# Performance work log

Hardware: AMD Instinct MI355X
Metric: run time of the kernel (lower is better)

Reference implementation:

```python
import jax, jax.numpy as jnp
import numpy as np

EPS = 1e-5


def _layer_norm(x, gamma, beta):
    mu = jnp.mean(x, axis=-1, keepdims=True)
    var = jnp.var(x, axis=-1, keepdims=True)
    return (x - mu) * jax.lax.rsqrt(var + EPS) * gamma + beta


def setup_inputs() -> dict:
    key = jax.random.key(0)
    B, I, H = 4096, 1024, 1024
    ks = jax.random.split(key, 6)
    x = jax.random.normal(ks[0], (B, I), dtype=jnp.float32)
    h = jax.random.normal(ks[1], (B, H), dtype=jnp.float32)
    c = jax.random.normal(ks[2], (B, H), dtype=jnp.float32)
    # nn.Linear(I+H, 4H): weight [4H, I+H], bias [4H]
    bound = 1.0 / np.sqrt(I + H)
    W = jax.random.uniform(ks[3], (4 * H, I + H), minval=-bound, maxval=bound, dtype=jnp.float32)
    b = jax.random.uniform(ks[4], (4 * H,), minval=-bound, maxval=bound, dtype=jnp.float32)
    inp = {"x": x, "h": h, "c": c, "W": W, "b": b}
    for name in ("i", "f", "g", "o", "c"):
        inp[f"ln_{name}_g"] = jnp.ones((H,), dtype=jnp.float32)
        inp[f"ln_{name}_b"] = jnp.zeros((H,), dtype=jnp.float32)
    return inp


def reference(x, h, c, W, b, ln_i_g, ln_i_b, ln_f_g, ln_f_b, ln_g_g, ln_g_b,
              ln_o_g, ln_o_b, ln_c_g, ln_c_b):
    H = h.shape[-1]
    xh = jnp.concatenate([x, h], axis=-1)              # [B, I+H]
    gates = xh @ W.T + b                               # [B, 4H]
    i_raw, f_raw, g_raw, o_raw = jnp.split(gates, 4, axis=-1)
    i = jax.nn.sigmoid(_layer_norm(i_raw, ln_i_g, ln_i_b))
    f = jax.nn.sigmoid(_layer_norm(f_raw, ln_f_g, ln_f_b))
    g = jnp.tanh(_layer_norm(g_raw, ln_g_g, ln_g_b))
    o = jax.nn.sigmoid(_layer_norm(o_raw, ln_o_g, ln_o_b))
    c_new = f * c + i * g
    h_new = o * jnp.tanh(_layer_norm(c_new, ln_c_g, ln_c_b))
    return (h_new, c_new)
```

## Files before the change

kernel.cpp:

```cpp
#include <hip/hip_runtime.h>
#include <hip/hip_bf16.h>

#define B_ROWS 4096
#define H_DIM  1024
#define K_DIM  2048
#define N_DIM  4096
#define NT     32

typedef __attribute__((ext_vector_type(8))) short bf16x8;
typedef __attribute__((ext_vector_type(4))) float f32x4;

__device__ __forceinline__ unsigned short f2bf(float f) {
  union { float f; unsigned int u; } v; v.f = f;
  unsigned int u = v.u;
  return (unsigned short)((u + 0x7fffu + ((u >> 16) & 1u)) >> 16);
}
__device__ __forceinline__ float bf2f(unsigned short u) {
  union { unsigned int u; float f; } v; v.u = ((unsigned int)u) << 16;
  return v.f;
}

__device__ __forceinline__ void gload_lds16(const void* g, void* l) {
  __builtin_amdgcn_global_load_lds(
      (const __attribute__((address_space(1))) void*)g,
      (__attribute__((address_space(3))) void*)l, 16, 0, 0);
}

__global__ __launch_bounds__(256) void pack_a_kernel(
    const float* __restrict__ x, const float* __restrict__ h,
    unsigned short* __restrict__ out) {
  int t = blockIdx.x * 256 + threadIdx.x;
  int e = t * 4;
  int row = e >> 11;
  int col = e & 2047;
  const float* src = (col < 1024) ? (x + (size_t)row * 1024 + col)
                                  : (h + (size_t)row * 1024 + (col - 1024));
  float4 v = *(const float4*)src;
  ushort4 o;
  o.x = f2bf(v.x); o.y = f2bf(v.y); o.z = f2bf(v.z); o.w = f2bf(v.w);
  *(ushort4*)(out + e) = o;
}

__global__ __launch_bounds__(256) void pack_w_kernel(
    const float* __restrict__ W, unsigned short* __restrict__ out) {
  int t = blockIdx.x * 256 + threadIdx.x;
  int e = t * 4;
  float4 v = *(const float4*)(W + e);
  ushort4 o;
  o.x = f2bf(v.x); o.y = f2bf(v.y); o.z = f2bf(v.z); o.w = f2bf(v.w);
  *(ushort4*)(out + e) = o;
}


#define STAGE(g, kt, dst) do {                              \
    gload_lds16((g) + (size_t)(kt) * 64, (dst));            \
    gload_lds16((g) + (size_t)(kt) * 64 + 32, (dst) + 1024); } while (0)

#define WAIT_LGKM0() do {                                   \
    asm volatile("s_waitcnt lgkmcnt(0)" ::: "memory");      \
    __builtin_amdgcn_sched_barrier(0); } while (0)

__global__ __launch_bounds__(512, 2) void gemm_kernel(
    const unsigned short* __restrict__ A, const unsigned short* __restrict__ W,
    const float* __restrict__ bias, unsigned short* __restrict__ C) {
  __shared__ __align__(16) char lds[131072];

  const int tid = threadIdx.x;
  const int w = tid >> 6, l = tid & 63;
  const int wm = w >> 2, wn = w & 3;
  const int bm = blockIdx.y * 256, bn = blockIdx.x * 256;

  const int lofs = (((l & 15) * 64) + ((l >> 4) * 16)) ^ ((l & 8) << 2);
  const int lane_r = (l >> 2) & 15;
  const int lane_c = ((l & 3) * 8) ^ (((l >> 5) & 1) * 16);

  const int rbA0 = w + (w & 4);
  const int rbA1 = rbA0 + 4;
  const int rbB0 = ((w >> 1) << 2) + (w & 1);
  const int rbB1 = rbB0 + 2;

  const unsigned short* gA0 = A + (size_t)(bm + rbA0 * 16 + lane_r) * K_DIM + lane_c;
  const unsigned short* gA1 = A + (size_t)(bm + rbA1 * 16 + lane_r) * K_DIM + lane_c;
  const unsigned short* gB0 = W + (size_t)(bn + rbB0 * 16 + lane_r) * K_DIM + lane_c;
  const unsigned short* gB1 = W + (size_t)(bn + rbB1 * 16 + lane_r) * K_DIM + lane_c;

  char* const L0 = lds;
  char* const L1 = lds + 65536;

  f32x4 acc[8][4];
#pragma unroll
  for (int i = 0; i < 8; ++i)
#pragma unroll
    for (int j = 0; j < 4; ++j) acc[i][j] = (f32x4)0.0f;

  STAGE(gA0, 0, L0 + rbA0 * 2048);
  STAGE(gB0, 0, L0 + 32768 + rbB0 * 2048);
  STAGE(gB1, 0, L0 + 32768 + rbB1 * 2048);
  STAGE(gA1, 0, L0 + rbA1 * 2048);
  STAGE(gA0, 1, L1 + rbA0 * 2048);
  STAGE(gB0, 1, L1 + 32768 + rbB0 * 2048);
  STAGE(gB1, 1, L1 + 32768 + rbB1 * 2048);
  asm volatile("s_waitcnt vmcnt(6)" ::: "memory");
  __builtin_amdgcn_s_barrier();

  bf16x8 a[4][2], b0[2][2], b1[2][2];

#pragma unroll 2
  for (int t = 0; t < NT; ++t) {
    const int buf = t & 1;
    char* const Lc = lds + buf * 65536;
    char* const Ln = lds + (buf ^ 1) * 65536;
    const char* const LA = Lc;
    const char* const LB = Lc + 32768;
    const int kt1 = (t + 1) & (NT - 1);
    const int kt2 = (t + 2) & (NT - 1);

#pragma unroll
    for (int mi = 0; mi < 4; ++mi)
#pragma unroll
      for (int kk = 0; kk < 2; ++kk)
        a[mi][kk] = *(const bf16x8*)(LA + (((wm * 8 + mi) * 2 + kk) << 10) + lofs);
#pragma unroll
    for (int ni = 0; ni < 2; ++ni)
#pragma unroll
      for (int kk = 0; kk < 2; ++kk)
        b0[ni][kk] = *(const bf16x8*)(LB + (((wn * 4 + ni) * 2 + kk) << 10) + lofs);
    STAGE(gA1, kt1, Ln + rbA1 * 2048);
    asm volatile("s_waitcnt lgkmcnt(8)" ::: "memory");
    __builtin_amdgcn_s_barrier();
    WAIT_LGKM0();
    __builtin_amdgcn_s_setprio(1);
#pragma unroll
    for (int mi = 0; mi < 4; ++mi)
#pragma unroll
      for (int ni = 0; ni < 2; ++ni)
#pragma unroll
        for (int kk = 0; kk < 2; ++kk)
          acc[mi][ni] = __builtin_amdgcn_mfma_f32_16x16x32_bf16(
              a[mi][kk], b0[ni][kk], acc[mi][ni], 0, 0, 0);
    __builtin_amdgcn_s_setprio(0);
    __builtin_amdgcn_s_barrier();

#pragma unroll
    for (int ni = 0; ni < 2; ++ni)
#pragma unroll
      for (int kk = 0; kk < 2; ++kk)
        b1[ni][kk] = *(const bf16x8*)(LB + (((wn * 4 + 2 + ni) * 2 + kk) << 10) + lofs);
    STAGE(gA0, kt2, Lc + rbA0 * 2048);
    __builtin_amdgcn_s_barrier();
    WAIT_LGKM0();
    __builtin_amdgcn_s_setprio(1);
#pragma unroll
    for (int mi = 0; mi < 4; ++mi)
#pragma unroll
      for (int ni = 0; ni < 2; ++ni)
#pragma unroll
        for (int kk = 0; kk < 2; ++kk)
          acc[mi][2 + ni] = __builtin_amdgcn_mfma_f32_16x16x32_bf16(
              a[mi][kk], b1[ni][kk], acc[mi][2 + ni], 0, 0, 0);
    __builtin_amdgcn_s_setprio(0);
    __builtin_amdgcn_s_barrier();

#pragma unroll
    for (int mi = 0; mi < 4; ++mi)
#pragma unroll
      for (int kk = 0; kk < 2; ++kk)
        a[mi][kk] = *(const bf16x8*)(LA + (((wm * 8 + 4 + mi) * 2 + kk) << 10) + lofs);
    STAGE(gB0, kt2, Lc + 32768 + rbB0 * 2048);
    __builtin_amdgcn_s_barrier();
    WAIT_LGKM0();
    __builtin_amdgcn_s_setprio(1);
#pragma unroll
    for (int mi = 0; mi < 4; ++mi)
#pragma unroll
      for (int ni = 0; ni < 2; ++ni)
#pragma unroll
        for (int kk = 0; kk < 2; ++kk)
          acc[4 + mi][2 + ni] = __builtin_amdgcn_mfma_f32_16x16x32_bf16(
              a[mi][kk], b1[ni][kk], acc[4 + mi][2 + ni], 0, 0, 0);
    __builtin_amdgcn_s_setprio(0);
    __builtin_amdgcn_s_barrier();

    STAGE(gB1, kt2, Lc + 32768 + rbB1 * 2048);
    asm volatile("s_waitcnt vmcnt(6)" ::: "memory");
    __builtin_amdgcn_s_barrier();
    __builtin_amdgcn_s_setprio(1);
#pragma unroll
    for (int mi = 0; mi < 4; ++mi)
#pragma unroll
      for (int ni = 0; ni < 2; ++ni)
#pragma unroll
        for (int kk = 0; kk < 2; ++kk)
          acc[4 + mi][ni] = __builtin_amdgcn_mfma_f32_16x16x32_bf16(
              a[mi][kk], b0[ni][kk], acc[4 + mi][ni], 0, 0, 0);
    __builtin_amdgcn_s_setprio(0);
    __builtin_amdgcn_s_barrier();
  }

  const int lm = l & 15, lq = l >> 4;
  float bv[4];
#pragma unroll
  for (int ni = 0; ni < 4; ++ni) bv[ni] = bias[bn + wn * 64 + ni * 16 + lm];
  unsigned short* Cb = C + (size_t)(bm + wm * 128) * N_DIM + bn + wn * 64;
#pragma unroll
  for (int mi = 0; mi < 8; ++mi)
#pragma unroll
    for (int j = 0; j < 4; ++j) {
      const size_t rofs = (size_t)(mi * 16 + lq * 4 + j) * N_DIM;
#pragma unroll
      for (int ni = 0; ni < 4; ++ni)
        Cb[rofs + ni * 16 + lm] = f2bf(acc[mi][ni][j] + bv[ni]);
    }
}

__device__ __forceinline__ float2 blk_sum2(float s, float q, float* red,
                                           int wid, int lane) {
#pragma unroll
  for (int o = 32; o >= 1; o >>= 1) {
    s += __shfl_xor(s, o, 64);
    q += __shfl_xor(q, o, 64);
  }
  __syncthreads();
  if (lane == 0) { red[wid * 2] = s; red[wid * 2 + 1] = q; }
  __syncthreads();
  s = red[0] + red[2] + red[4] + red[6];
  q = red[1] + red[3] + red[5] + red[7];
  return make_float2(s, q);
}

__device__ __forceinline__ float sigmoidf_(float x) {
  return 1.0f / (1.0f + __expf(-x));
}
__device__ __forceinline__ float tanhf_(float x) {
  return 1.0f - 2.0f / (__expf(2.0f * x) + 1.0f);
}

__global__ __launch_bounds__(256) void ln_lstm_kernel(
    const unsigned short* __restrict__ gates, const float* __restrict__ cprev,
    const float* __restrict__ g_i, const float* __restrict__ b_i,
    const float* __restrict__ g_f, const float* __restrict__ b_f,
    const float* __restrict__ g_g, const float* __restrict__ b_g,
    const float* __restrict__ g_o, const float* __restrict__ b_o,
    const float* __restrict__ g_c, const float* __restrict__ b_c,
    float* __restrict__ out) {
  const int b = blockIdx.x;
  const int t = threadIdx.x;
  const int wid = t >> 6, lane = t & 63;
  __shared__ float red[8];

  const unsigned short* grow = gates + (size_t)b * N_DIM;
  const int c0 = t * 4;

  float v[4][4];
#pragma unroll
  for (int g = 0; g < 4; g++) {
    ushort4 raw = *(const ushort4*)(grow + g * 1024 + c0);
    v[g][0] = bf2f(raw.x); v[g][1] = bf2f(raw.y);
    v[g][2] = bf2f(raw.z); v[g][3] = bf2f(raw.w);
  }

  const float4 gamma[4] = {*(const float4*)(g_i + c0), *(const float4*)(g_f + c0),
                           *(const float4*)(g_g + c0), *(const float4*)(g_o + c0)};
  const float4 beta[4]  = {*(const float4*)(b_i + c0), *(const float4*)(b_f + c0),
                           *(const float4*)(b_g + c0), *(const float4*)(b_o + c0)};

  float a[4][4];
#pragma unroll
  for (int g = 0; g < 4; g++) {
    float s = v[g][0] + v[g][1] + v[g][2] + v[g][3];
    float q = v[g][0]*v[g][0] + v[g][1]*v[g][1] + v[g][2]*v[g][2] + v[g][3]*v[g][3];
    float2 r = blk_sum2(s, q, red, wid, lane);
    float mu = r.x * (1.0f / 1024.0f);
    float var = r.y * (1.0f / 1024.0f) - mu * mu;
    float inv = rsqrtf(var + 1e-5f);
    const float* gm = (const float*)&gamma[g];
    const float* bt = (const float*)&beta[g];
#pragma unroll
    for (int j = 0; j < 4; j++) {
      float n = (v[g][j] - mu) * inv * gm[j] + bt[j];
      a[g][j] = (g == 2) ? tanhf_(n) : sigmoidf_(n);
    }
  }

  float4 cp = *(const float4*)(cprev + (size_t)b * 1024 + c0);
  const float* cpe = (const float*)&cp;
  float cn[4];
#pragma unroll
  for (int j = 0; j < 4; j++)
    cn[j] = a[1][j] * cpe[j] + a[0][j] * a[2][j];

  {
    float s = cn[0] + cn[1] + cn[2] + cn[3];
    float q = cn[0]*cn[0] + cn[1]*cn[1] + cn[2]*cn[2] + cn[3]*cn[3];
    float2 r = blk_sum2(s, q, red, wid, lane);
    float mu = r.x * (1.0f / 1024.0f);
    float var = r.y * (1.0f / 1024.0f) - mu * mu;
    float inv = rsqrtf(var + 1e-5f);
    float4 gm = *(const float4*)(g_c + c0);
    float4 bt = *(const float4*)(b_c + c0);
    const float* gme = (const float*)&gm;
    const float* bte = (const float*)&bt;
    float hn[4];
#pragma unroll
    for (int j = 0; j < 4; j++) {
      float n = (cn[j] - mu) * inv * gme[j] + bte[j];
      hn[j] = a[3][j] * tanhf_(n);
    }
    *(float4*)(out + (size_t)b * 1024 + c0) = make_float4(hn[0], hn[1], hn[2], hn[3]);
    *(float4*)(out + (size_t)B_ROWS * H_DIM + (size_t)b * 1024 + c0) =
        make_float4(cn[0], cn[1], cn[2], cn[3]);
  }
}

extern "C" void kernel_launch(void* const* d_in, const int* in_sizes, int n_in,
                              void* d_out, int out_size, void* d_ws,
                              size_t ws_size, hipStream_t stream) {
  const float* x    = (const float*)d_in[0];
  const float* h    = (const float*)d_in[1];
  const float* c    = (const float*)d_in[2];
  const float* W    = (const float*)d_in[3];
  const float* bias = (const float*)d_in[4];
  const float* ln_i_g = (const float*)d_in[5];
  const float* ln_i_b = (const float*)d_in[6];
  const float* ln_f_g = (const float*)d_in[7];
  const float* ln_f_b = (const float*)d_in[8];
  const float* ln_g_g = (const float*)d_in[9];
  const float* ln_g_b = (const float*)d_in[10];
  const float* ln_o_g = (const float*)d_in[11];
  const float* ln_o_b = (const float*)d_in[12];
  const float* ln_c_g = (const float*)d_in[13];
  const float* ln_c_b = (const float*)d_in[14];

  unsigned short* Abf = (unsigned short*)d_ws;
  unsigned short* Wbf = Abf + (size_t)B_ROWS * K_DIM;
  unsigned short* gates = Wbf + (size_t)N_DIM * K_DIM;

  pack_a_kernel<<<(B_ROWS * K_DIM) / (4 * 256), 256, 0, stream>>>(x, h, Abf);
  pack_w_kernel<<<(N_DIM * K_DIM) / (4 * 256), 256, 0, stream>>>(W, Wbf);

  dim3 ggrid(N_DIM / 256, B_ROWS / 256);
  gemm_kernel<<<ggrid, 512, 0, stream>>>(Abf, Wbf, bias, gates);

  ln_lstm_kernel<<<B_ROWS, 256, 0, stream>>>(
      gates, c, ln_i_g, ln_i_b, ln_f_g, ln_f_b, ln_g_g, ln_g_b,
      ln_o_g, ln_o_b, ln_c_g, ln_c_b, (float*)d_out);
}
```

Baseline: 104.6 us.

## Prefetch next-tile LDS fragments into double registers and merge pack kernels

```diff
diff --git a/kernel.cpp b/kernel.cpp
--- a/kernel.cpp
+++ b/kernel.cpp
@@ -26,29 +26,30 @@
       (__attribute__((address_space(3))) void*)l, 16, 0, 0);
 }
 
-__global__ __launch_bounds__(256) void pack_a_kernel(
+__global__ __launch_bounds__(256) void pack_kernel(
     const float* __restrict__ x, const float* __restrict__ h,
-    unsigned short* __restrict__ out) {
-  int t = blockIdx.x * 256 + threadIdx.x;
-  int e = t * 4;
-  int row = e >> 11;
-  int col = e & 2047;
-  const float* src = (col < 1024) ? (x + (size_t)row * 1024 + col)
-                                  : (h + (size_t)row * 1024 + (col - 1024));
-  float4 v = *(const float4*)src;
-  ushort4 o;
-  o.x = f2bf(v.x); o.y = f2bf(v.y); o.z = f2bf(v.z); o.w = f2bf(v.w);
-  *(ushort4*)(out + e) = o;
-}
-
-__global__ __launch_bounds__(256) void pack_w_kernel(
-    const float* __restrict__ W, unsigned short* __restrict__ out) {
-  int t = blockIdx.x * 256 + threadIdx.x;
-  int e = t * 4;
-  float4 v = *(const float4*)(W + e);
-  ushort4 o;
-  o.x = f2bf(v.x); o.y = f2bf(v.y); o.z = f2bf(v.z); o.w = f2bf(v.w);
-  *(ushort4*)(out + e) = o;
+    const float* __restrict__ W, unsigned short* __restrict__ Abf,
+    unsigned short* __restrict__ Wbf) {
+  int bid = blockIdx.x;
+  if (bid < 8192) {
+    int t = bid * 256 + threadIdx.x;
+    int e = t * 4;
+    int row = e >> 11;
+    int col = e & 2047;
+    const float* src = (col < 1024) ? (x + (size_t)row * 1024 + col)
+                                    : (h + (size_t)row * 1024 + (col - 1024));
+    float4 v = *(const float4*)src;
+    ushort4 o;
+    o.x = f2bf(v.x); o.y = f2bf(v.y); o.z = f2bf(v.z); o.w = f2bf(v.w);
+    *(ushort4*)(Abf + e) = o;
+  } else {
+    int t = (bid - 8192) * 256 + threadIdx.x;
+    int e = t * 4;
+    float4 v = *(const float4*)(W + e);
+    ushort4 o;
+    o.x = f2bf(v.x); o.y = f2bf(v.y); o.z = f2bf(v.z); o.w = f2bf(v.w);
+    *(ushort4*)(Wbf + e) = o;
+  }
 }
 
 
@@ -103,7 +104,18 @@
   asm volatile("s_waitcnt vmcnt(6)" ::: "memory");
   __builtin_amdgcn_s_barrier();
 
-  bf16x8 a[4][2], b0[2][2], b1[2][2];
+  bf16x8 a0[4][2], a1[4][2], b0[2][2], b1[2][2];
+
+#pragma unroll
+  for (int mi = 0; mi < 4; ++mi)
+#pragma unroll
+    for (int kk = 0; kk < 2; ++kk)
+      a0[mi][kk] = *(const bf16x8*)(L0 + (((wm * 8 + mi) * 2 + kk) << 10) + lofs);
+#pragma unroll
+  for (int ni = 0; ni < 2; ++ni)
+#pragma unroll
+    for (int kk = 0; kk < 2; ++kk)
+      b0[ni][kk] = *(const bf16x8*)(L0 + 32768 + (((wn * 4 + ni) * 2 + kk) << 10) + lofs);
 
 #pragma unroll 2
   for (int t = 0; t < NT; ++t) {
@@ -112,40 +124,31 @@
     char* const Ln = lds + (buf ^ 1) * 65536;
     const char* const LA = Lc;
     const char* const LB = Lc + 32768;
+    const char* const LAn = Ln;
+    const char* const LBn = Ln + 32768;
     const int kt1 = (t + 1) & (NT - 1);
     const int kt2 = (t + 2) & (NT - 1);
 
-#pragma unroll
-    for (int mi = 0; mi < 4; ++mi)
-#pragma unroll
-      for (int kk = 0; kk < 2; ++kk)
-        a[mi][kk] = *(const bf16x8*)(LA + (((wm * 8 + mi) * 2 + kk) << 10) + lofs);
-#pragma unroll
-    for (int ni = 0; ni < 2; ++ni)
-#pragma unroll
-      for (int kk = 0; kk < 2; ++kk)
-        b0[ni][kk] = *(const bf16x8*)(LB + (((wn * 4 + ni) * 2 + kk) << 10) + lofs);
     STAGE(gA1, kt1, Ln + rbA1 * 2048);
-    asm volatile("s_waitcnt lgkmcnt(8)" ::: "memory");
     __builtin_amdgcn_s_barrier();
     WAIT_LGKM0();
     __builtin_amdgcn_s_setprio(1);
 #pragma unroll
+    for (int ni = 0; ni < 2; ++ni)
+#pragma unroll
+      for (int kk = 0; kk < 2; ++kk)
+        b1[ni][kk] = *(const bf16x8*)(LB + (((wn * 4 + 2 + ni) * 2 + kk) << 10) + lofs);
+#pragma unroll
     for (int mi = 0; mi < 4; ++mi)
 #pragma unroll
       for (int ni = 0; ni < 2; ++ni)
 #pragma unroll
         for (int kk = 0; kk < 2; ++kk)
           acc[mi][ni] = __builtin_amdgcn_mfma_f32_16x16x32_bf16(
-              a[mi][kk], b0[ni][kk], acc[mi][ni], 0, 0, 0);
+              a0[mi][kk], b0[ni][kk], acc[mi][ni], 0, 0, 0);
     __builtin_amdgcn_s_setprio(0);
     __builtin_amdgcn_s_barrier();
 
-#pragma unroll
-    for (int ni = 0; ni < 2; ++ni)
-#pragma unroll
-      for (int kk = 0; kk < 2; ++kk)
-        b1[ni][kk] = *(const bf16x8*)(LB + (((wn * 4 + 2 + ni) * 2 + kk) << 10) + lofs);
     STAGE(gA0, kt2, Lc + rbA0 * 2048);
     __builtin_amdgcn_s_barrier();
     WAIT_LGKM0();
@@ -153,19 +156,19 @@
 #pragma unroll
     for (int mi = 0; mi < 4; ++mi)
 #pragma unroll
+      for (int kk = 0; kk < 2; ++kk)
+        a1[mi][kk] = *(const bf16x8*)(LA + (((wm * 8 + 4 + mi) * 2 + kk) << 10) + lofs);
+#pragma unroll
+    for (int mi = 0; mi < 4; ++mi)
+#pragma unroll
       for (int ni = 0; ni < 2; ++ni)
 #pragma unroll
         for (int kk = 0; kk < 2; ++kk)
           acc[mi][2 + ni] = __builtin_amdgcn_mfma_f32_16x16x32_bf16(
-              a[mi][kk], b1[ni][kk], acc[mi][2 + ni], 0, 0, 0);
+              a0[mi][kk], b1[ni][kk], acc[mi][2 + ni], 0, 0, 0);
     __builtin_amdgcn_s_setprio(0);
     __builtin_amdgcn_s_barrier();
 
-#pragma unroll
-    for (int mi = 0; mi < 4; ++mi)
-#pragma unroll
-      for (int kk = 0; kk < 2; ++kk)
-        a[mi][kk] = *(const bf16x8*)(LA + (((wm * 8 + 4 + mi) * 2 + kk) << 10) + lofs);
     STAGE(gB0, kt2, Lc + 32768 + rbB0 * 2048);
     __builtin_amdgcn_s_barrier();
     WAIT_LGKM0();
@@ -177,7 +180,7 @@
 #pragma unroll
         for (int kk = 0; kk < 2; ++kk)
           acc[4 + mi][2 + ni] = __builtin_amdgcn_mfma_f32_16x16x32_bf16(
-              a[mi][kk], b1[ni][kk], acc[4 + mi][2 + ni], 0, 0, 0);
+              a1[mi][kk], b1[ni][kk], acc[4 + mi][2 + ni], 0, 0, 0);
     __builtin_amdgcn_s_setprio(0);
     __builtin_amdgcn_s_barrier();
 
@@ -192,8 +195,18 @@
 #pragma unroll
         for (int kk = 0; kk < 2; ++kk)
           acc[4 + mi][ni] = __builtin_amdgcn_mfma_f32_16x16x32_bf16(
-              a[mi][kk], b0[ni][kk], acc[4 + mi][ni], 0, 0, 0);
+              a1[mi][kk], b0[ni][kk], acc[4 + mi][ni], 0, 0, 0);
     __builtin_amdgcn_s_setprio(0);
+#pragma unroll
+    for (int mi = 0; mi < 4; ++mi)
+#pragma unroll
+      for (int kk = 0; kk < 2; ++kk)
+        a0[mi][kk] = *(const bf16x8*)(LAn + (((wm * 8 + mi) * 2 + kk) << 10) + lofs);
+#pragma unroll
+    for (int ni = 0; ni < 2; ++ni)
+#pragma unroll
+      for (int kk = 0; kk < 2; ++kk)
+        b0[ni][kk] = *(const bf16x8*)(LBn + (((wn * 4 + ni) * 2 + kk) << 10) + lofs);
     __builtin_amdgcn_s_barrier();
   }
 
@@ -335,8 +348,7 @@
   unsigned short* Wbf = Abf + (size_t)B_ROWS * K_DIM;
   unsigned short* gates = Wbf + (size_t)N_DIM * K_DIM;
 
-  pack_a_kernel<<<(B_ROWS * K_DIM) / (4 * 256), 256, 0, stream>>>(x, h, Abf);
-  pack_w_kernel<<<(N_DIM * K_DIM) / (4 * 256), 256, 0, stream>>>(W, Wbf);
+  pack_kernel<<<16384, 256, 0, stream>>>(x, h, W, Abf, Wbf);
 
   dim3 ggrid(N_DIM / 256, B_ROWS / 256);
   gemm_kernel<<<ggrid, 512, 0, stream>>>(Abf, Wbf, bias, gates);
```

Result: no change. 102.8 us (-1.7%).
